# Performance work log

Measured on AMD Instinct MI355X. Metric: run time of the kernel, lower is better.

The kernel has to match this reference:

```python
import jax, jax.numpy as jnp
import numpy as np

B = 65536
KC = 64   # n_coarse
KF = 64   # n_fine (n_fine_depth = 0)
HID = 32
NEAR, FAR = 2.0, 6.0


def setup_inputs() -> dict:
    key = jax.random.key(0)
    ks = jax.random.split(key, 8)
    origins = jax.random.normal(ks[0], (B, 3), jnp.float32) * 0.1
    dirs = jax.random.normal(ks[1], (B, 3), jnp.float32)
    dirs = dirs / jnp.linalg.norm(dirs, axis=-1, keepdims=True)
    near = jnp.full((B, 1), NEAR, jnp.float32)
    far = jnp.full((B, 1), FAR, jnp.float32)
    rays = jnp.concatenate([origins, dirs, near, far], axis=-1)  # (B, 8)
    u_coarse = jax.random.uniform(ks[2], (B, KC), jnp.float32)
    u_fine = jax.random.uniform(ks[3], (B, KF), jnp.float32)
    u_jitter = jax.random.uniform(ks[4], (B, KF), jnp.float32)
    W1 = jax.random.normal(ks[5], (3, HID), jnp.float32) * 0.5
    b1 = jnp.zeros((HID,), jnp.float32)
    W2 = jax.random.normal(ks[6], (HID, 4), jnp.float32) * 0.5
    b2 = jnp.zeros((4,), jnp.float32)
    return {"rays": rays, "u_coarse": u_coarse, "u_fine": u_fine,
            "u_jitter": u_jitter, "W1": W1, "b1": b1, "W2": W2, "b2": b2}


def _mlp(points, W1, b1, W2, b2):
    # points: (B, K, 3) -> rgb (B, K, 3) in [0,1], sigma (B, K)
    h = jax.nn.relu(jnp.einsum("bkd,dh->bkh", points, W1) + b1)
    o = jnp.einsum("bkh,hc->bkc", h, W2) + b2
    return jax.nn.sigmoid(o[..., :3]), o[..., 3]


def _composite(rays, z_samp, W1, b1, W2, b2):
    # deltas between consecutive samples; last delta up to `far`
    deltas = jnp.concatenate(
        [z_samp[:, 1:] - z_samp[:, :-1], rays[:, -1:] - z_samp[:, -1:]], axis=-1)  # (B, K)
    points = rays[:, None, :3] + z_samp[..., None] * rays[:, None, 3:6]  # (B, K, 3)
    rgbs, sigmas = _mlp(points, W1, b1, W2, b2)
    alphas = 1.0 - jnp.exp(-deltas * jax.nn.relu(sigmas))  # (B, K)
    alphas_shifted = jnp.concatenate(
        [jnp.ones_like(alphas[:, :1]), 1.0 - alphas + 1e-10], axis=-1)
    T = jnp.cumprod(alphas_shifted, axis=-1)  # (B, K+1)
    weights = alphas * T[:, :-1]  # (B, K)
    rgb_final = jnp.sum(weights[..., None] * rgbs, axis=1)  # (B, 3)
    depth_final = jnp.sum(weights * z_samp, axis=1)  # (B,)
    return weights, rgb_final, depth_final


def _sample_coarse(rays, u_coarse):
    near, far = rays[:, -2:-1], rays[:, -1:]
    step = 1.0 / KC
    z_steps = jnp.linspace(0.0, 1.0 - step, KC, dtype=jnp.float32)[None, :] + u_coarse * step
    return near * (1.0 - z_steps) + far * z_steps  # (B, KC), lindisp=False


def _sample_fine(rays, weights, u_fine, u_jitter):
    # inverse-CDF importance sampling; weights are detached in the original
    w = jax.lax.stop_gradient(weights) + 1e-5
    pdf = w / jnp.sum(w, axis=-1, keepdims=True)
    cdf = jnp.cumsum(pdf, axis=-1)
    cdf = jnp.concatenate([jnp.zeros_like(cdf[:, :1]), cdf], axis=-1)  # (B, KC+1)
    inds = jax.vmap(lambda c, u: jnp.searchsorted(c, u, side="right"))(cdf, u_fine)
    inds = jnp.maximum(inds.astype(jnp.float32) - 1.0, 0.0)
    z_steps = (inds + u_jitter) / KC
    near, far = rays[:, -2:-1], rays[:, -1:]
    return near * (1.0 - z_steps) + far * z_steps  # (B, KF)


def reference(rays, u_coarse, u_fine, u_jitter, W1, b1, W2, b2):
    z_coarse = _sample_coarse(rays, u_coarse)
    weights_c, rgb_c, depth_c = _composite(rays, z_coarse, W1, b1, W2, b2)
    z_fine = _sample_fine(rays, weights_c, u_fine, u_jitter)
    z_comb = jnp.sort(jnp.concatenate([z_coarse, z_fine], axis=-1), axis=-1)  # (B, KC+KF)
    weights_f, rgb_f, depth_f = _composite(rays, z_comb, W1, b1, W2, b2)
    return jnp.concatenate(
        [rgb_f, depth_f[:, None], rgb_c, depth_c[:, None]], axis=-1)  # (B, 8)
```

## Files before the change

### kernel.cpp

```cpp
#include <hip/hip_runtime.h>
#include <math.h>


typedef float f32x2 __attribute__((ext_vector_type(2)));
typedef _Float16 f16x2v __attribute__((ext_vector_type(2)));
typedef _Float16 f16x4v __attribute__((ext_vector_type(4)));

__device__ __forceinline__ float fast_rcp(float x) { return __builtin_amdgcn_rcpf(x); }
__device__ __forceinline__ float fsigmoid(float x) { return fast_rcp(1.0f + __expf(-x)); }

__device__ __forceinline__ f32x2 splat_lo(f32x2 v) { return __builtin_shufflevector(v, v, 0, 0); }
__device__ __forceinline__ f32x2 splat_hi(f32x2 v) { return __builtin_shufflevector(v, v, 1, 1); }

__device__ __forceinline__ void wave_fence() {
    asm volatile("" ::: "memory");
    __builtin_amdgcn_wave_barrier();
}

template <int CTRL, int RMASK>
__device__ __forceinline__ float dpp_f(float x, float oldv) {
    return __int_as_float(__builtin_amdgcn_update_dpp(
        __float_as_int(oldv), __float_as_int(x), CTRL, RMASK, 0xf, false));
}
template <int CTRL, int RMASK>
__device__ __forceinline__ int dpp_i(int x, int oldv) {
    return __builtin_amdgcn_update_dpp(oldv, x, CTRL, RMASK, 0xf, false);
}

__device__ __forceinline__ float scan_mul(float x) {
    x *= dpp_f<0x111, 0xf>(x, 1.0f);
    x *= dpp_f<0x112, 0xf>(x, 1.0f);
    x *= dpp_f<0x114, 0xf>(x, 1.0f);
    x *= dpp_f<0x118, 0xf>(x, 1.0f);
    x *= dpp_f<0x142, 0xa>(x, 1.0f);
    x *= dpp_f<0x143, 0xc>(x, 1.0f);
    return x;
}
__device__ __forceinline__ float scan_add(float x) {
    x += dpp_f<0x111, 0xf>(x, 0.0f);
    x += dpp_f<0x112, 0xf>(x, 0.0f);
    x += dpp_f<0x114, 0xf>(x, 0.0f);
    x += dpp_f<0x118, 0xf>(x, 0.0f);
    x += dpp_f<0x142, 0xa>(x, 0.0f);
    x += dpp_f<0x143, 0xc>(x, 0.0f);
    return x;
}
__device__ __forceinline__ int scan_add_i(int x) {
    x += dpp_i<0x111, 0xf>(x, 0);
    x += dpp_i<0x112, 0xf>(x, 0);
    x += dpp_i<0x114, 0xf>(x, 0);
    x += dpp_i<0x118, 0xf>(x, 0);
    x += dpp_i<0x142, 0xa>(x, 0);
    x += dpp_i<0x143, 0xc>(x, 0);
    return x;
}

__global__ __launch_bounds__(256) void nerf_render(
    const float* __restrict__ rays,
    const float* __restrict__ u_coarse,
    const float* __restrict__ u_fine,
    const float* __restrict__ u_jitter,
    const float* __restrict__ W1,
    const float* __restrict__ b1,
    const float* __restrict__ W2,
    const float* __restrict__ b2,
    float* __restrict__ out)
{
    __shared__ float  acS[4][64];
    __shared__ float  zM[4][128];
    __shared__ f16x2v rgM[4][128];
    __shared__ f16x2v bsM[4][128];

    const int lane = threadIdx.x & 63;
    const int wv   = threadIdx.x >> 6;
    const int ray  = (blockIdx.x << 2) + wv;

    const float* rp = rays + ray * 8;
    const float ox = rp[0], oy = rp[1], oz = rp[2];
    const float ddx = rp[3], ddy = rp[4], ddz = rp[5];
    const float nearv = rp[6], farv = rp[7];

    {
        const int j = lane & 31;
        const float w0 = W1[j], w1 = W1[32 + j], w2 = W1[64 + j];
        const bool isA = lane < 32;
        const float px = isA ? ox : ddx;
        const float py = isA ? oy : ddy;
        const float pz = isA ? oz : ddz;
        const float bb = isA ? b1[j] : 0.0f;
        acS[wv][lane] = fmaf(px, w0, fmaf(py, w1, fmaf(pz, w2, bb)));
    }
    wave_fence();

    const float* aw = &acS[wv][0];
    const float* cw = &acS[wv][32];

    auto mlp = [&](float z, float& rr, float& gg, float& bb_, float& sg) {
        const f32x2 zz = {z, z};
        const f32x2 zero2 = {0.0f, 0.0f};
        f32x2 acc01 = *reinterpret_cast<const f32x2*>(b2);
        f32x2 acc23 = *reinterpret_cast<const f32x2*>(b2 + 2);
#pragma unroll
        for (int j = 0; j < 32; j += 4) {
            const f32x2 a01 = *reinterpret_cast<const f32x2*>(aw + j);
            const f32x2 a23 = *reinterpret_cast<const f32x2*>(aw + j + 2);
            const f32x2 c01 = *reinterpret_cast<const f32x2*>(cw + j);
            const f32x2 c23 = *reinterpret_cast<const f32x2*>(cw + j + 2);
            f32x2 h01 = __builtin_elementwise_fma(zz, c01, a01);
            f32x2 h23 = __builtin_elementwise_fma(zz, c23, a23);
            h01 = __builtin_elementwise_max(h01, zero2);
            h23 = __builtin_elementwise_max(h23, zero2);
            {
                const f32x2 wA = *reinterpret_cast<const f32x2*>(W2 + (j + 0) * 4);
                const f32x2 wB = *reinterpret_cast<const f32x2*>(W2 + (j + 0) * 4 + 2);
                const f32x2 hs = splat_lo(h01);
                acc01 = __builtin_elementwise_fma(hs, wA, acc01);
                acc23 = __builtin_elementwise_fma(hs, wB, acc23);
            }
            {
                const f32x2 wA = *reinterpret_cast<const f32x2*>(W2 + (j + 1) * 4);
                const f32x2 wB = *reinterpret_cast<const f32x2*>(W2 + (j + 1) * 4 + 2);
                const f32x2 hs = splat_hi(h01);
                acc01 = __builtin_elementwise_fma(hs, wA, acc01);
                acc23 = __builtin_elementwise_fma(hs, wB, acc23);
            }
            {
                const f32x2 wA = *reinterpret_cast<const f32x2*>(W2 + (j + 2) * 4);
                const f32x2 wB = *reinterpret_cast<const f32x2*>(W2 + (j + 2) * 4 + 2);
                const f32x2 hs = splat_lo(h23);
                acc01 = __builtin_elementwise_fma(hs, wA, acc01);
                acc23 = __builtin_elementwise_fma(hs, wB, acc23);
            }
            {
                const f32x2 wA = *reinterpret_cast<const f32x2*>(W2 + (j + 3) * 4);
                const f32x2 wB = *reinterpret_cast<const f32x2*>(W2 + (j + 3) * 4 + 2);
                const f32x2 hs = splat_hi(h23);
                acc01 = __builtin_elementwise_fma(hs, wA, acc01);
                acc23 = __builtin_elementwise_fma(hs, wB, acc23);
            }
        }
        rr = fsigmoid(acc01.x); gg = fsigmoid(acc01.y);
        bb_ = fsigmoid(acc23.x); sg = acc23.y;
    };

    const float uc = u_coarse[ray * 64 + lane];
    const float zsc = (float)lane * 0.015625f + uc * 0.015625f;
    const float zc = nearv * (1.0f - zsc) + farv * zsc;

    const float zcn = dpp_f<0x130, 0xf>(zc, zc);
    const float deltac = (lane == 63) ? (farv - zc) : (zcn - zc);

    float cr_, cg_, cb_, csig;
    mlp(zc, cr_, cg_, cb_, csig);
    const float alphac = 1.0f - __expf(-deltac * fmaxf(csig, 0.0f));
    const float sc = 1.0f - alphac + 1e-10f;

    const float pincl = scan_mul(sc);
    const float Tc = dpp_f<0x138, 0xf>(pincl, 1.0f);
    const float wc = alphac * Tc;

    const float rc = scan_add(wc * cr_);
    const float gc = scan_add(wc * cg_);
    const float bc = scan_add(wc * cb_);
    const float dc = scan_add(wc * zc);

    const float wp = wc + 1e-5f;
    const float cdf = scan_add(wp);
    const float tot = __int_as_float(__builtin_amdgcn_readlane(__float_as_int(cdf), 63));

    const float uf = u_fine[ray * 64 + lane] * tot;
    int cnt = 0;
#pragma unroll
    for (int step = 64; step >= 1; step >>= 1) {
        const int idx = cnt + step - 1;
        const float v = __shfl(cdf, idx < 64 ? idx : 63);
        if (idx < 64 && v <= uf) cnt += step;
    }
    const float uj = u_jitter[ray * 64 + lane];
    float key = (float)cnt + uj;

#pragma unroll
    for (int k = 2; k <= 64; k <<= 1) {
#pragma unroll
        for (int j = k >> 1; j > 0; j >>= 1) {
            float v;
            if (j == 1)      v = dpp_f<0xB1, 0xf>(key, key);
            else if (j == 2) v = dpp_f<0x4E, 0xf>(key, key);
            else             v = __shfl_xor(key, j);
            const bool keepMin = (((lane & j) == 0) == ((lane & k) == 0));
            key = keepMin ? fminf(key, v) : fmaxf(key, v);
        }
    }

    int cnti = (int)key; cnti = cnti > 63 ? 63 : cnti;
    const float ujr = key - (float)cnti;
    const float ucv = __shfl(uc, cnti);
    const int g = cnti + ((ucv <= ujr) ? 1 : 0);
    const int pos_f = lane + g;

    unsigned int* hist = reinterpret_cast<unsigned int*>(&zM[wv][0]);
    hist[lane] = 0u;
    wave_fence();
    atomicAdd(&hist[g], 1u);
    wave_fence();
    const int cfv = scan_add_i((int)hist[lane]);
    const int pos_c = lane + cfv;
    wave_fence();

    const float zsf = key * 0.015625f;
    const float zf = nearv * (1.0f - zsf) + farv * zsf;
    float fr_, fg_, fb_, fsig;
    mlp(zf, fr_, fg_, fb_, fsig);

    {
        zM[wv][pos_c] = zc;
        zM[wv][pos_f] = zf;
        f16x2v t;
        t.x = (_Float16)cr_;  t.y = (_Float16)cg_;  rgM[wv][pos_c] = t;
        t.x = (_Float16)fr_;  t.y = (_Float16)fg_;  rgM[wv][pos_f] = t;
        t.x = (_Float16)cb_;  t.y = (_Float16)csig; bsM[wv][pos_c] = t;
        t.x = (_Float16)fb_;  t.y = (_Float16)fsig; bsM[wv][pos_f] = t;
    }
    wave_fence();

    const float2 zz2 = *reinterpret_cast<const float2*>(&zM[wv][2 * lane]);
    const float z0 = zz2.x, z1 = zz2.y;
    const float z2n = zM[wv][(2 * lane + 2) & 127];
    const f16x4v rg4 = *reinterpret_cast<const f16x4v*>(&rgM[wv][2 * lane]);
    const f16x4v bs4 = *reinterpret_cast<const f16x4v*>(&bsM[wv][2 * lane]);
    const float r0 = (float)rg4.x, g0 = (float)rg4.y;
    const float r1 = (float)rg4.z, g1 = (float)rg4.w;
    const float b0 = (float)bs4.x, s0 = (float)bs4.y;
    const float b1v = (float)bs4.z, s1 = (float)bs4.w;

    const float d0 = z1 - z0;
    const float d1 = (lane == 63) ? (farv - z1) : (z2n - z1);

    const float al0 = 1.0f - __expf(-d0 * fmaxf(s0, 0.0f));
    const float al1 = 1.0f - __expf(-d1 * fmaxf(s1, 0.0f));
    const float t0 = 1.0f - al0 + 1e-10f;
    const float t1 = 1.0f - al1 + 1e-10f;

    const float ppincl = scan_mul(t0 * t1);
    const float Te = dpp_f<0x138, 0xf>(ppincl, 1.0f);
    const float w0 = al0 * Te;
    const float w1 = al1 * (Te * t0);

    const float fr = scan_add(fmaf(w0, r0, w1 * r1));
    const float fg = scan_add(fmaf(w0, g0, w1 * g1));
    const float fb = scan_add(fmaf(w0, b0, w1 * b1v));
    const float fd = scan_add(fmaf(w0, z0, w1 * z1));

    if (lane == 63) {
        float4* op = reinterpret_cast<float4*>(out + ray * 8);
        op[0] = make_float4(fr, fg, fb, fd);
        op[1] = make_float4(rc, gc, bc, dc);
    }
}

extern "C" void kernel_launch(void* const* d_in, const int* in_sizes, int n_in,
                              void* d_out, int out_size, void* d_ws, size_t ws_size,
                              hipStream_t stream) {
    const float* rays     = (const float*)d_in[0];
    const float* u_coarse = (const float*)d_in[1];
    const float* u_fine   = (const float*)d_in[2];
    const float* u_jitter = (const float*)d_in[3];
    const float* W1       = (const float*)d_in[4];
    const float* b1       = (const float*)d_in[5];
    const float* W2       = (const float*)d_in[6];
    const float* b2       = (const float*)d_in[7];
    float* out = (float*)d_out;

    const int B = in_sizes[0] / 8;
    dim3 grid(B / 4), block(256);
    hipLaunchKernelGGL(nerf_render, grid, block, 0, stream,
                       rays, u_coarse, u_fine, u_jitter, W1, b1, W2, b2, out);
}
```

Measured before the change: 81.07 us.

## Use transposed quad reductions, LDS-staged W2, swizzles, and a shorter search

The four separate 64-lane scans per composite are replaced by a transposed quad reduction that packs r/g/b/depth into lanes and reduces them together. This cuts the number of cross-lane steps. W2 is staged once per block in LDS, which needs a block barrier instead of a wave fence. Bitonic-sort exchanges at distances 4/8/16 use ds_swizzle instead of generic shuffles, and the binary search drops its redundant first step and bounds checks. The exp is reused for both alpha and transmittance, and the output is written by eight lanes.

```diff
diff --git a/kernel.cpp b/kernel.cpp
--- a/kernel.cpp
+++ b/kernel.cpp
@@ -25,6 +25,10 @@
 template <int CTRL, int RMASK>
 __device__ __forceinline__ int dpp_i(int x, int oldv) {
     return __builtin_amdgcn_update_dpp(oldv, x, CTRL, RMASK, 0xf, false);
+}
+template <int OFF>
+__device__ __forceinline__ float swz_f(float x) {
+    return __int_as_float(__builtin_amdgcn_ds_swizzle(__float_as_int(x), OFF));
 }
 
 __device__ __forceinline__ float scan_mul(float x) {
@@ -52,6 +56,22 @@
     x += dpp_i<0x118, 0xf>(x, 0);
     x += dpp_i<0x142, 0xa>(x, 0);
     x += dpp_i<0x143, 0xc>(x, 0);
+    return x;
+}
+
+__device__ __forceinline__ float quad_reduce4(float v0, float v1, float v2, float v3, int lane) {
+    const bool b0 = (lane & 1) != 0;
+    const float w01 = b0 ? v0 : v1, k01 = b0 ? v1 : v0;
+    const float x01 = k01 + dpp_f<0xB1, 0xf>(w01, w01);
+    const float w23 = b0 ? v2 : v3, k23 = b0 ? v3 : v2;
+    const float x23 = k23 + dpp_f<0xB1, 0xf>(w23, w23);
+    const bool b1 = (lane & 2) != 0;
+    const float w = b1 ? x01 : x23, k = b1 ? x23 : x01;
+    float x = k + dpp_f<0x4E, 0xf>(w, w);
+    x += dpp_f<0x124, 0xf>(x, x);
+    x += dpp_f<0x128, 0xf>(x, x);
+    x += swz_f<0x401F>(x);
+    x += __shfl_xor(x, 32);
     return x;
 }
 
@@ -66,6 +86,7 @@
     const float* __restrict__ b2,
     float* __restrict__ out)
 {
+    __shared__ f32x2  w2S[64];
     __shared__ float  acS[4][64];
     __shared__ float  zM[4][128];
     __shared__ f16x2v rgM[4][128];
@@ -79,6 +100,8 @@
     const float ox = rp[0], oy = rp[1], oz = rp[2];
     const float ddx = rp[3], ddy = rp[4], ddz = rp[5];
     const float nearv = rp[6], farv = rp[7];
+
+    if (threadIdx.x < 64) w2S[threadIdx.x] = reinterpret_cast<const f32x2*>(W2)[threadIdx.x];
 
     {
         const int j = lane & 31;
@@ -90,7 +113,7 @@
         const float bb = isA ? b1[j] : 0.0f;
         acS[wv][lane] = fmaf(px, w0, fmaf(py, w1, fmaf(pz, w2, bb)));
     }
-    wave_fence();
+    __syncthreads();
 
     const float* aw = &acS[wv][0];
     const float* cw = &acS[wv][32];
@@ -111,29 +134,25 @@
             h01 = __builtin_elementwise_max(h01, zero2);
             h23 = __builtin_elementwise_max(h23, zero2);
             {
-                const f32x2 wA = *reinterpret_cast<const f32x2*>(W2 + (j + 0) * 4);
-                const f32x2 wB = *reinterpret_cast<const f32x2*>(W2 + (j + 0) * 4 + 2);
+                const f32x2 wA = w2S[(j + 0) * 2], wB = w2S[(j + 0) * 2 + 1];
                 const f32x2 hs = splat_lo(h01);
                 acc01 = __builtin_elementwise_fma(hs, wA, acc01);
                 acc23 = __builtin_elementwise_fma(hs, wB, acc23);
             }
             {
-                const f32x2 wA = *reinterpret_cast<const f32x2*>(W2 + (j + 1) * 4);
-                const f32x2 wB = *reinterpret_cast<const f32x2*>(W2 + (j + 1) * 4 + 2);
+                const f32x2 wA = w2S[(j + 1) * 2], wB = w2S[(j + 1) * 2 + 1];
                 const f32x2 hs = splat_hi(h01);
                 acc01 = __builtin_elementwise_fma(hs, wA, acc01);
                 acc23 = __builtin_elementwise_fma(hs, wB, acc23);
             }
             {
-                const f32x2 wA = *reinterpret_cast<const f32x2*>(W2 + (j + 2) * 4);
-                const f32x2 wB = *reinterpret_cast<const f32x2*>(W2 + (j + 2) * 4 + 2);
+                const f32x2 wA = w2S[(j + 2) * 2], wB = w2S[(j + 2) * 2 + 1];
                 const f32x2 hs = splat_lo(h23);
                 acc01 = __builtin_elementwise_fma(hs, wA, acc01);
                 acc23 = __builtin_elementwise_fma(hs, wB, acc23);
             }
             {
-                const f32x2 wA = *reinterpret_cast<const f32x2*>(W2 + (j + 3) * 4);
-                const f32x2 wB = *reinterpret_cast<const f32x2*>(W2 + (j + 3) * 4 + 2);
+                const f32x2 wA = w2S[(j + 3) * 2], wB = w2S[(j + 3) * 2 + 1];
                 const f32x2 hs = splat_hi(h23);
                 acc01 = __builtin_elementwise_fma(hs, wA, acc01);
                 acc23 = __builtin_elementwise_fma(hs, wB, acc23);
@@ -152,17 +171,15 @@
 
     float cr_, cg_, cb_, csig;
     mlp(zc, cr_, cg_, cb_, csig);
-    const float alphac = 1.0f - __expf(-deltac * fmaxf(csig, 0.0f));
-    const float sc = 1.0f - alphac + 1e-10f;
+    const float ec = __expf(-deltac * fmaxf(csig, 0.0f));
+    const float alphac = 1.0f - ec;
+    const float sc = ec + 1e-10f;
 
     const float pincl = scan_mul(sc);
     const float Tc = dpp_f<0x138, 0xf>(pincl, 1.0f);
     const float wc = alphac * Tc;
 
-    const float rc = scan_add(wc * cr_);
-    const float gc = scan_add(wc * cg_);
-    const float bc = scan_add(wc * cb_);
-    const float dc = scan_add(wc * zc);
+    const float coarseTot = quad_reduce4(wc * cr_, wc * cg_, wc * cb_, wc * zc, lane);
 
     const float wp = wc + 1e-5f;
     const float cdf = scan_add(wp);
@@ -171,10 +188,9 @@
     const float uf = u_fine[ray * 64 + lane] * tot;
     int cnt = 0;
 #pragma unroll
-    for (int step = 64; step >= 1; step >>= 1) {
-        const int idx = cnt + step - 1;
-        const float v = __shfl(cdf, idx < 64 ? idx : 63);
-        if (idx < 64 && v <= uf) cnt += step;
+    for (int step = 32; step >= 1; step >>= 1) {
+        const float v = __shfl(cdf, cnt + step - 1);
+        if (v <= uf) cnt += step;
     }
     const float uj = u_jitter[ray * 64 + lane];
     float key = (float)cnt + uj;
@@ -184,9 +200,12 @@
 #pragma unroll
         for (int j = k >> 1; j > 0; j >>= 1) {
             float v;
-            if (j == 1)      v = dpp_f<0xB1, 0xf>(key, key);
-            else if (j == 2) v = dpp_f<0x4E, 0xf>(key, key);
-            else             v = __shfl_xor(key, j);
+            if (j == 1)       v = dpp_f<0xB1, 0xf>(key, key);
+            else if (j == 2)  v = dpp_f<0x4E, 0xf>(key, key);
+            else if (j == 4)  v = swz_f<0x101F>(key);
+            else if (j == 8)  v = swz_f<0x201F>(key);
+            else if (j == 16) v = swz_f<0x401F>(key);
+            else              v = __shfl_xor(key, 32);
             const bool keepMin = (((lane & j) == 0) == ((lane & k) == 0));
             key = keepMin ? fminf(key, v) : fmaxf(key, v);
         }
@@ -236,25 +255,23 @@
     const float d0 = z1 - z0;
     const float d1 = (lane == 63) ? (farv - z1) : (z2n - z1);
 
-    const float al0 = 1.0f - __expf(-d0 * fmaxf(s0, 0.0f));
-    const float al1 = 1.0f - __expf(-d1 * fmaxf(s1, 0.0f));
-    const float t0 = 1.0f - al0 + 1e-10f;
-    const float t1 = 1.0f - al1 + 1e-10f;
+    const float e0 = __expf(-d0 * fmaxf(s0, 0.0f));
+    const float e1 = __expf(-d1 * fmaxf(s1, 0.0f));
+    const float al0 = 1.0f - e0;
+    const float al1 = 1.0f - e1;
+    const float t0 = e0 + 1e-10f;
+    const float t1 = e1 + 1e-10f;
 
     const float ppincl = scan_mul(t0 * t1);
     const float Te = dpp_f<0x138, 0xf>(ppincl, 1.0f);
     const float w0 = al0 * Te;
     const float w1 = al1 * (Te * t0);
 
-    const float fr = scan_add(fmaf(w0, r0, w1 * r1));
-    const float fg = scan_add(fmaf(w0, g0, w1 * g1));
-    const float fb = scan_add(fmaf(w0, b0, w1 * b1v));
-    const float fd = scan_add(fmaf(w0, z0, w1 * z1));
-
-    if (lane == 63) {
-        float4* op = reinterpret_cast<float4*>(out + ray * 8);
-        op[0] = make_float4(fr, fg, fb, fd);
-        op[1] = make_float4(rc, gc, bc, dc);
+    const float fineTot = quad_reduce4(fmaf(w0, r0, w1 * r1), fmaf(w0, g0, w1 * g1),
+                                       fmaf(w0, b0, w1 * b1v), fmaf(w0, z0, w1 * z1), lane);
+
+    if (lane < 8) {
+        out[ray * 8 + lane] = (lane < 4) ? fineTot : coarseTot;
     }
 }
 
```

Measured after the change: 75.14 us. -7.3%, faster.
